# Kernel optimization log

Measured on AMD Instinct MI355X. Metric: run time of the kernel, lower is better.

## Reference

```python
import jax, jax.numpy as jnp
import numpy as np

N = 100_000      # nodes
E = 1_600_000    # edges (avg degree 16)
D_IN, D_HID, D_OUT = 64, 64, 10


def setup_inputs() -> dict:
    key = jax.random.key(0)
    ks = jax.random.split(key, 9)
    x = jax.random.normal(ks[0], (N, D_IN), jnp.float32)
    edge_index = jax.random.randint(ks[1], (2, E), 0, N, dtype=jnp.int32)

    def lin(k, i, o):
        # Glorot-ish init for a Linear(i, o) weight, stored as (in, out)
        return jax.random.normal(k, (i, o), jnp.float32) / np.sqrt(i).astype(np.float32)

    return dict(
        x=x, edge_index=edge_index,
        W_out0=lin(ks[2], D_IN, D_HID), b0=jnp.zeros((D_HID,), jnp.float32), W_root0=lin(ks[3], D_IN, D_HID),
        W_out1=lin(ks[4], D_HID, D_HID), b1=jnp.zeros((D_HID,), jnp.float32), W_root1=lin(ks[5], D_HID, D_HID),
        W_out2=lin(ks[6], D_HID, D_OUT), b2=jnp.zeros((D_OUT,), jnp.float32), W_root2=lin(ks[7], D_HID, D_OUT),
    )


def _cluster_gcn_conv(x, src, dst, deg_inv, W_out, b, W_root):
    # PyG ClusterGCNConv (add_self_loops=False, diag_lambda=0):
    #   agg[i] = (1/deg_in(i)) * sum_{(j->i) in E} x[j]
    #   out    = agg @ W_out + b + x @ W_root
    agg = jax.ops.segment_sum(x[src], dst, num_segments=N)  # [N, d]
    agg = agg * deg_inv[:, None]
    return agg @ W_out + b + x @ W_root


def reference(x, edge_index, W_out0, b0, W_root0, W_out1, b1, W_root1, W_out2, b2, W_root2):
    src, dst = edge_index[0], edge_index[1]
    deg = jax.ops.segment_sum(jnp.ones((E,), x.dtype), dst, num_segments=N)
    deg_inv = 1.0 / jnp.clip(deg, 1.0)  # degree(col).clamp_(1.)

    h = jax.nn.relu(_cluster_gcn_conv(x, src, dst, deg_inv, W_out0, b0, W_root0))
    # dropout(p=0.5) is identity in eval mode (reference uses eval semantics)
    h = jax.nn.relu(_cluster_gcn_conv(h, src, dst, deg_inv, W_out1, b1, W_root1))
    h = _cluster_gcn_conv(h, src, dst, deg_inv, W_out2, b2, W_root2)
    return jax.nn.log_softmax(h, axis=-1)
```

## Files before the change

### kernel.cpp

```cpp
#include <hip/hip_runtime.h>
#include <hip/hip_bf16.h>
#include <math.h>

#define N_NODES 100000
#define N_EDGES 1600000
#define D 64
#define DOUT 10
#define CAP 64
#define APAD 136
#define NBIN 782
#define ABLK 256
#define ACHUNK 6272
#define SCAP 32

typedef __attribute__((ext_vector_type(8))) short short8;
typedef __attribute__((ext_vector_type(4))) float f32x4;

__device__ __forceinline__ unsigned short f2bf(float f) {
    __hip_bfloat16 h = __float2bfloat16(f);
    return __builtin_bit_cast(unsigned short, h);
}
__device__ __forceinline__ float blo(unsigned v) { return __builtin_bit_cast(float, v << 16); }
__device__ __forceinline__ float bhi(unsigned v) { return __builtin_bit_cast(float, v & 0xFFFF0000u); }

#define PROCE(dv, sv) { int bin = (dv) >> 7; int r = atomicAdd(&hist[bin], 1); \
    if (r < SCAP) ebuf[((size_t)blk * NBIN + bin) * SCAP + r] = ((sv) << 7) | ((dv) & 127); }

__global__ __launch_bounds__(1024) void partA_kernel(
    const int* __restrict__ src, const int* __restrict__ dst,
    int* __restrict__ ebuf, int* __restrict__ counts,
    const float* __restrict__ x, unsigned short* __restrict__ xb,
    const float* __restrict__ W_out0, const float* __restrict__ W_root0,
    const float* __restrict__ W_out1, const float* __restrict__ W_root1,
    const float* __restrict__ W_out2, const float* __restrict__ W_root2,
    unsigned short* __restrict__ Wt0, unsigned short* __restrict__ Wt1,
    unsigned short* __restrict__ Wt2) {
    __shared__ int hist[NBIN];
    int tid = threadIdx.x;
    int blk = blockIdx.x;
    for (int i = tid; i < NBIN; i += 1024) hist[i] = 0;
    __syncthreads();
    int e0 = blk * ACHUNK;
    for (int b = tid; b < ACHUNK / 4; b += 1024) {
        int e = e0 + b * 4;
        if (e + 4 <= N_EDGES) {
            int4 d4 = *(const int4*)&dst[e];
            int4 s4 = *(const int4*)&src[e];
            PROCE(d4.x, s4.x) PROCE(d4.y, s4.y) PROCE(d4.z, s4.z) PROCE(d4.w, s4.w)
        } else {
            for (int k = 0; e + k < N_EDGES && k < 4; ++k) {
                int dv = dst[e + k], sv = src[e + k];
                PROCE(dv, sv)
            }
        }
    }
    __syncthreads();
    for (int i = tid; i < NBIN; i += 1024) {
        int h = hist[i];
        counts[blk * NBIN + i] = h < SCAP ? h : SCAP;
    }

    const int CTOT = (N_NODES + 1) * D / 4;
    for (int i = blk * 1024 + tid; i < CTOT; i += ABLK * 1024) {
        ushort4 o;
        if (i * 4 < N_NODES * D) {
            float4 v = *(const float4*)&x[i * 4];
            o.x = f2bf(v.x); o.y = f2bf(v.y); o.z = f2bf(v.z); o.w = f2bf(v.w);
        } else {
            o.x = 0; o.y = 0; o.z = 0; o.w = 0;
        }
        *(ushort4*)&xb[i * 4] = o;
    }

    for (int idx = blk * 1024 + tid; idx < 16384 + 2048; idx += ABLK * 1024) {
        if (idx < 8192) {
            int j = idx >> 7, k = idx & 127;
            Wt0[idx] = f2bf(k < 64 ? W_out0[k * D + j] : W_root0[(k - 64) * D + j]);
        } else if (idx < 16384) {
            int t = idx - 8192;
            int j = t >> 7, k = t & 127;
            Wt1[t] = f2bf(k < 64 ? W_out1[k * D + j] : W_root1[(k - 64) * D + j]);
        } else {
            int t = idx - 16384;
            int j = t >> 7, k = t & 127;
            float v = 0.f;
            if (j < DOUT) v = k < 64 ? W_out2[k * DOUT + j] : W_root2[(k - 64) * DOUT + j];
            Wt2[t] = f2bf(v);
        }
    }
}

__global__ __launch_bounds__(256) void partB_kernel(const int* __restrict__ ebuf,
                                                    const int* __restrict__ counts,
                                                    int* __restrict__ cnt,
                                                    int* __restrict__ bucket) {
    __shared__ int lb[128 * CAP];
    __shared__ int lcnt[128];
    __shared__ int sc[ABLK];
    int tid = threadIdx.x;
    int bin = blockIdx.x;
    for (int i = tid; i < 128 * CAP; i += 256) lb[i] = N_NODES;
    if (tid < 128) lcnt[tid] = 0;
    if (tid < ABLK) sc[tid] = counts[tid * NBIN + bin];
    __syncthreads();
    for (int i = tid; i < ABLK * SCAP; i += 256) {
        int seg = i >> 5;
        int slot = i & (SCAP - 1);
        if (slot < sc[seg]) {
            int v = ebuf[((size_t)seg * NBIN + bin) * SCAP + slot];
            int dloc = v & 127;
            int p = atomicAdd(&lcnt[dloc], 1);
            if (p < CAP) lb[dloc * CAP + p] = v >> 7;
        }
    }
    __syncthreads();
    size_t nodeBase = (size_t)bin << 7;
    int lastNode = N_NODES - (int)nodeBase;
    for (int i = tid; i < 128 * CAP / 4; i += 256) {
        int dloc = (i * 4) >> 6;
        if (dloc < lastNode)
            *(int4*)&bucket[nodeBase * CAP + i * 4] = *(const int4*)&lb[i * 4];
    }
    if (tid < 128 && tid < lastNode) cnt[nodeBase + tid] = lcnt[tid];
}

__global__ __launch_bounds__(256) void gather_kernel(
    const unsigned short* __restrict__ in, unsigned short* __restrict__ agg,
    const int* __restrict__ cnt, const int* __restrict__ bucket) {
    int tid = threadIdx.x;
    int lane = tid & 63;
    int g = lane >> 3, j = lane & 7;
    int wv = (blockIdx.x * blockDim.x + tid) >> 6;
    int nw = (gridDim.x * blockDim.x) >> 6;
    const int NP = (N_NODES + 8) / 8;

    for (int pr = wv; pr < NP; pr += nw) {
        int n0 = pr * 8;
        int nd = n0 + g;
        int node = nd < N_NODES ? nd : 0;
        int c = nd < N_NODES ? cnt[nd] : 0;
        int cc = c < CAP ? c : CAP;
        const int* __restrict__ brow = &bucket[(size_t)node * CAP];

        float a0 = 0.f, a1 = 0.f, a2 = 0.f, a3 = 0.f,
              a4 = 0.f, a5 = 0.f, a6 = 0.f, a7 = 0.f;
        uint4 rA = {0, 0, 0, 0}, rB = {0, 0, 0, 0}, rC = {0, 0, 0, 0};
        if (cc > 0) rA = *(const uint4*)&in[(size_t)brow[0] * D + j * 8];
        if (cc > 1) rB = *(const uint4*)&in[(size_t)brow[1] * D + j * 8];
        if (cc > 2) rC = *(const uint4*)&in[(size_t)brow[2] * D + j * 8];
        for (int it = 0; it < cc; ++it) {
            uint4 r = rA;
            rA = rB; rB = rC;
            if (it + 3 < cc) rC = *(const uint4*)&in[(size_t)brow[it + 3] * D + j * 8];
            a0 += blo(r.x); a1 += bhi(r.x);
            a2 += blo(r.y); a3 += bhi(r.y);
            a4 += blo(r.z); a5 += bhi(r.z);
            a6 += blo(r.w); a7 += bhi(r.w);
        }
        if (nd <= N_NODES) {
            float dinv = 1.0f / (float)(c > 0 ? c : 1);
            uint4 pk;
            pk.x = (unsigned)f2bf(a0 * dinv) | ((unsigned)f2bf(a1 * dinv) << 16);
            pk.y = (unsigned)f2bf(a2 * dinv) | ((unsigned)f2bf(a3 * dinv) << 16);
            pk.z = (unsigned)f2bf(a4 * dinv) | ((unsigned)f2bf(a5 * dinv) << 16);
            pk.w = (unsigned)f2bf(a6 * dinv) | ((unsigned)f2bf(a7 * dinv) << 16);
            *(uint4*)&agg[(size_t)nd * D + j * 8] = pk;
        }
    }
}

__global__ __launch_bounds__(256) void gemm_hidden_kernel(
    const unsigned short* __restrict__ agg, const unsigned short* __restrict__ xin,
    unsigned short* __restrict__ out, const unsigned short* __restrict__ Wt_g,
    const float* __restrict__ bias_v) {
    __shared__ __align__(16) unsigned short Wt[64 * APAD];
    int tid = threadIdx.x;
#pragma unroll
    for (int i = 0; i < 4; ++i) {
        int e = (tid + i * 256) * 8;
        uint4 v = *(const uint4*)&Wt_g[e];
        *(uint4*)&Wt[(e >> 7) * APAD + (e & 127)] = v;
    }
    __syncthreads();

    int lane = tid & 63, w = tid >> 6;
    int r16 = lane & 15, g4 = lane >> 4;
    int base = blockIdx.x * 64;
    int arow = base + w * 16 + r16;
    int nd = arow < N_NODES ? arow : N_NODES;

    f32x4 acc[4] = {{0.f,0.f,0.f,0.f},{0.f,0.f,0.f,0.f},{0.f,0.f,0.f,0.f},{0.f,0.f,0.f,0.f}};
#pragma unroll
    for (int ks = 0; ks < 4; ++ks) {
        int koff = ks * 32 + g4 * 8;
        short8 a;
        if (ks < 2) a = *(const short8*)&agg[(size_t)nd * D + koff];
        else        a = *(const short8*)&xin[(size_t)nd * D + (koff - 64)];
#pragma unroll
        for (int n = 0; n < 4; ++n) {
            short8 b = *(const short8*)&Wt[(n * 16 + r16) * APAD + koff];
            acc[n] = __builtin_amdgcn_mfma_f32_16x16x32_bf16(a, b, acc[n], 0, 0, 0);
        }
    }
#pragma unroll
    for (int n = 0; n < 4; ++n) {
        int col = n * 16 + r16;
        float bias = bias_v[col];
#pragma unroll
        for (int r = 0; r < 4; ++r) {
            int node = base + w * 16 + g4 * 4 + r;
            if (node <= N_NODES) {
                float v = node < N_NODES ? fmaxf(acc[n][r] + bias, 0.f) : 0.f;
                out[(size_t)node * D + col] = f2bf(v);
            }
        }
    }
}

__global__ __launch_bounds__(256) void gemm_out_kernel(
    const unsigned short* __restrict__ agg, const unsigned short* __restrict__ xin,
    float* __restrict__ out, const unsigned short* __restrict__ Wt_g,
    const float* __restrict__ bias_v) {
    __shared__ __align__(16) unsigned short Wt[16 * APAD];
    int tid = threadIdx.x;
    {
        int e = tid * 8;
        uint4 v = *(const uint4*)&Wt_g[e];
        *(uint4*)&Wt[(e >> 7) * APAD + (e & 127)] = v;
    }
    __syncthreads();

    int lane = tid & 63, w = tid >> 6;
    int r16 = lane & 15, g4 = lane >> 4;
    int base = blockIdx.x * 64;
    int arow = base + w * 16 + r16;
    int nd = arow < N_NODES ? arow : N_NODES;

    f32x4 acc = {0.f, 0.f, 0.f, 0.f};
#pragma unroll
    for (int ks = 0; ks < 4; ++ks) {
        int koff = ks * 32 + g4 * 8;
        short8 a;
        if (ks < 2) a = *(const short8*)&agg[(size_t)nd * D + koff];
        else        a = *(const short8*)&xin[(size_t)nd * D + (koff - 64)];
        short8 b = *(const short8*)&Wt[r16 * APAD + koff];
        acc = __builtin_amdgcn_mfma_f32_16x16x32_bf16(a, b, acc, 0, 0, 0);
    }
    float bias = r16 < DOUT ? bias_v[r16] : -1e30f;
#pragma unroll
    for (int r = 0; r < 4; ++r) {
        float v = acc[r] + bias;
        float m = v;
        m = fmaxf(m, __shfl_xor(m, 1, 16));
        m = fmaxf(m, __shfl_xor(m, 2, 16));
        m = fmaxf(m, __shfl_xor(m, 4, 16));
        m = fmaxf(m, __shfl_xor(m, 8, 16));
        float e = expf(v - m);
        float s = e;
        s += __shfl_xor(s, 1, 16);
        s += __shfl_xor(s, 2, 16);
        s += __shfl_xor(s, 4, 16);
        s += __shfl_xor(s, 8, 16);
        int node = base + w * 16 + g4 * 4 + r;
        if (node < N_NODES && r16 < DOUT)
            out[(size_t)node * DOUT + r16] = v - m - logf(s);
    }
}

extern "C" void kernel_launch(void* const* d_in, const int* in_sizes, int n_in,
                              void* d_out, int out_size, void* d_ws, size_t ws_size,
                              hipStream_t stream) {
    const float* x       = (const float*)d_in[0];
    const int*   ei      = (const int*)d_in[1];
    const int*   src     = ei;
    const int*   dst     = ei + N_EDGES;
    const float* W_out0  = (const float*)d_in[2];
    const float* b0      = (const float*)d_in[3];
    const float* W_root0 = (const float*)d_in[4];
    const float* W_out1  = (const float*)d_in[5];
    const float* b1      = (const float*)d_in[6];
    const float* W_root1 = (const float*)d_in[7];
    const float* W_out2  = (const float*)d_in[8];
    const float* b2      = (const float*)d_in[9];
    const float* W_root2 = (const float*)d_in[10];
    float* outp = (float*)d_out;

    const size_t ROWS = (size_t)(N_NODES + 1) * D;
    unsigned short* xb  = (unsigned short*)d_ws;
    unsigned short* h0  = xb + ROWS;
    unsigned short* h1  = h0 + ROWS;
    unsigned short* Wt0 = h1 + ROWS;
    unsigned short* Wt1 = Wt0 + 8192;
    unsigned short* Wt2 = Wt1 + 8192;
    int* cnt    = (int*)(Wt2 + 2048);
    int* bucket = cnt + N_NODES;
    int* ebuf   = bucket + (size_t)N_NODES * CAP;
    int* counts = ebuf + (size_t)ABLK * NBIN * SCAP;

    partA_kernel<<<ABLK, 1024, 0, stream>>>(src, dst, ebuf, counts, x, xb,
                                            W_out0, W_root0, W_out1, W_root1,
                                            W_out2, W_root2, Wt0, Wt1, Wt2);
    partB_kernel<<<NBIN, 256, 0, stream>>>(ebuf, counts, cnt, bucket);

    const int GB = 2048;
    const int tiles = (N_NODES + 63) / 64;
    gather_kernel<<<GB, 256, 0, stream>>>(xb, h1, cnt, bucket);
    gemm_hidden_kernel<<<tiles, 256, 0, stream>>>(h1, xb, h0, Wt0, b0);
    gather_kernel<<<GB, 256, 0, stream>>>(h0, xb, cnt, bucket);
    gemm_hidden_kernel<<<tiles, 256, 0, stream>>>(xb, h0, h1, Wt1, b1);
    gather_kernel<<<GB, 256, 0, stream>>>(h1, h0, cnt, bucket);
    gemm_out_kernel<<<tiles, 256, 0, stream>>>(h0, h1, outp, Wt2, b2);
}
```

Before: 277.3 us.

## Fuse neighbor gather into per-layer GEMM kernels via LDS staging

Merges the separate gather and GEMM kernels of each layer into one kernel per layer. Each block gathers and mean-aggregates its 64 nodes' neighbor features straight into shared memory next to the root features, then runs the MFMA GEMM from LDS. This removes the write and re-read of the intermediate aggregate buffer and three kernel launches. In exchange, the gather parallelism is tied to the GEMM tile grid (one block per 64 nodes) and each block uses more LDS, which could lower occupancy.

```diff
diff --git a/kernel.cpp b/kernel.cpp
--- a/kernel.cpp
+++ b/kernel.cpp
@@ -124,78 +124,70 @@
     if (tid < 128 && tid < lastNode) cnt[nodeBase + tid] = lcnt[tid];
 }
 
-__global__ __launch_bounds__(256) void gather_kernel(
-    const unsigned short* __restrict__ in, unsigned short* __restrict__ agg,
-    const int* __restrict__ cnt, const int* __restrict__ bucket) {
-    int tid = threadIdx.x;
-    int lane = tid & 63;
-    int g = lane >> 3, j = lane & 7;
-    int wv = (blockIdx.x * blockDim.x + tid) >> 6;
-    int nw = (gridDim.x * blockDim.x) >> 6;
-    const int NP = (N_NODES + 8) / 8;
-
-    for (int pr = wv; pr < NP; pr += nw) {
-        int n0 = pr * 8;
-        int nd = n0 + g;
-        int node = nd < N_NODES ? nd : 0;
-        int c = nd < N_NODES ? cnt[nd] : 0;
-        int cc = c < CAP ? c : CAP;
-        const int* __restrict__ brow = &bucket[(size_t)node * CAP];
-
-        float a0 = 0.f, a1 = 0.f, a2 = 0.f, a3 = 0.f,
-              a4 = 0.f, a5 = 0.f, a6 = 0.f, a7 = 0.f;
-        uint4 rA = {0, 0, 0, 0}, rB = {0, 0, 0, 0}, rC = {0, 0, 0, 0};
-        if (cc > 0) rA = *(const uint4*)&in[(size_t)brow[0] * D + j * 8];
-        if (cc > 1) rB = *(const uint4*)&in[(size_t)brow[1] * D + j * 8];
-        if (cc > 2) rC = *(const uint4*)&in[(size_t)brow[2] * D + j * 8];
-        for (int it = 0; it < cc; ++it) {
-            uint4 r = rA;
-            rA = rB; rB = rC;
-            if (it + 3 < cc) rC = *(const uint4*)&in[(size_t)brow[it + 3] * D + j * 8];
-            a0 += blo(r.x); a1 += bhi(r.x);
-            a2 += blo(r.y); a3 += bhi(r.y);
-            a4 += blo(r.z); a5 += bhi(r.z);
-            a6 += blo(r.w); a7 += bhi(r.w);
-        }
-        if (nd <= N_NODES) {
-            float dinv = 1.0f / (float)(c > 0 ? c : 1);
-            uint4 pk;
-            pk.x = (unsigned)f2bf(a0 * dinv) | ((unsigned)f2bf(a1 * dinv) << 16);
-            pk.y = (unsigned)f2bf(a2 * dinv) | ((unsigned)f2bf(a3 * dinv) << 16);
-            pk.z = (unsigned)f2bf(a4 * dinv) | ((unsigned)f2bf(a5 * dinv) << 16);
-            pk.w = (unsigned)f2bf(a6 * dinv) | ((unsigned)f2bf(a7 * dinv) << 16);
-            *(uint4*)&agg[(size_t)nd * D + j * 8] = pk;
-        }
-    }
-}
-
-__global__ __launch_bounds__(256) void gemm_hidden_kernel(
-    const unsigned short* __restrict__ agg, const unsigned short* __restrict__ xin,
-    unsigned short* __restrict__ out, const unsigned short* __restrict__ Wt_g,
-    const float* __restrict__ bias_v) {
+
+#define GATHER_TO_LDS(p)                                                              \
+    {                                                                                 \
+        int nl = w * 16 + (p) * 8 + g;                                                \
+        int nd = base + nl;                                                           \
+        int node = nd < N_NODES ? nd : 0;                                             \
+        int c = nd < N_NODES ? cnt[nd] : 0;                                           \
+        int cc = c < CAP ? c : CAP;                                                   \
+        const int* __restrict__ brow = &bucket[(size_t)node * CAP];                   \
+        float a0 = 0.f, a1 = 0.f, a2 = 0.f, a3 = 0.f,                                 \
+              a4 = 0.f, a5 = 0.f, a6 = 0.f, a7 = 0.f;                                 \
+        uint4 rA = {0,0,0,0}, rB = {0,0,0,0}, rC = {0,0,0,0};                         \
+        if (cc > 0) rA = *(const uint4*)&in[(size_t)brow[0] * D + j * 8];             \
+        if (cc > 1) rB = *(const uint4*)&in[(size_t)brow[1] * D + j * 8];             \
+        if (cc > 2) rC = *(const uint4*)&in[(size_t)brow[2] * D + j * 8];             \
+        for (int it = 0; it < cc; ++it) {                                             \
+            uint4 r = rA;                                                             \
+            rA = rB; rB = rC;                                                         \
+            if (it + 3 < cc) rC = *(const uint4*)&in[(size_t)brow[it + 3] * D + j * 8]; \
+            a0 += blo(r.x); a1 += bhi(r.x);                                           \
+            a2 += blo(r.y); a3 += bhi(r.y);                                           \
+            a4 += blo(r.z); a5 += bhi(r.z);                                           \
+            a6 += blo(r.w); a7 += bhi(r.w);                                           \
+        }                                                                             \
+        float dinv = 1.0f / (float)(c > 0 ? c : 1);                                   \
+        uint4 pk;                                                                     \
+        pk.x = (unsigned)f2bf(a0 * dinv) | ((unsigned)f2bf(a1 * dinv) << 16);         \
+        pk.y = (unsigned)f2bf(a2 * dinv) | ((unsigned)f2bf(a3 * dinv) << 16);         \
+        pk.z = (unsigned)f2bf(a4 * dinv) | ((unsigned)f2bf(a5 * dinv) << 16);         \
+        pk.w = (unsigned)f2bf(a6 * dinv) | ((unsigned)f2bf(a7 * dinv) << 16);         \
+        *(uint4*)&A[nl * APAD + j * 8] = pk;                                          \
+    }
+
+__global__ __launch_bounds__(256) void layer_fused_kernel(
+    const unsigned short* __restrict__ in, unsigned short* __restrict__ out,
+    const int* __restrict__ cnt, const int* __restrict__ bucket,
+    const unsigned short* __restrict__ Wt_g, const float* __restrict__ bias_v) {
+    __shared__ __align__(16) unsigned short A[64 * APAD];
     __shared__ __align__(16) unsigned short Wt[64 * APAD];
     int tid = threadIdx.x;
 #pragma unroll
     for (int i = 0; i < 4; ++i) {
         int e = (tid + i * 256) * 8;
-        uint4 v = *(const uint4*)&Wt_g[e];
-        *(uint4*)&Wt[(e >> 7) * APAD + (e & 127)] = v;
-    }
-    __syncthreads();
-
+        *(uint4*)&Wt[(e >> 7) * APAD + (e & 127)] = *(const uint4*)&Wt_g[e];
+    }
+    int base = blockIdx.x * 64;
+    for (int idx = tid; idx < 512; idx += 256) {
+        int r = idx >> 3, ch = idx & 7;
+        int nd = base + r; if (nd > N_NODES) nd = N_NODES;
+        *(uint4*)&A[r * APAD + D + ch * 8] = *(const uint4*)&in[(size_t)nd * D + ch * 8];
+    }
     int lane = tid & 63, w = tid >> 6;
+    int g = lane >> 3, j = lane & 7;
+    GATHER_TO_LDS(0)
+    GATHER_TO_LDS(1)
+    __syncthreads();
+
     int r16 = lane & 15, g4 = lane >> 4;
-    int base = blockIdx.x * 64;
-    int arow = base + w * 16 + r16;
-    int nd = arow < N_NODES ? arow : N_NODES;
-
+    int arow = w * 16 + r16;
     f32x4 acc[4] = {{0.f,0.f,0.f,0.f},{0.f,0.f,0.f,0.f},{0.f,0.f,0.f,0.f},{0.f,0.f,0.f,0.f}};
 #pragma unroll
     for (int ks = 0; ks < 4; ++ks) {
         int koff = ks * 32 + g4 * 8;
-        short8 a;
-        if (ks < 2) a = *(const short8*)&agg[(size_t)nd * D + koff];
-        else        a = *(const short8*)&xin[(size_t)nd * D + (koff - 64)];
+        short8 a = *(const short8*)&A[arow * APAD + koff];
 #pragma unroll
         for (int n = 0; n < 4; ++n) {
             short8 b = *(const short8*)&Wt[(n * 16 + r16) * APAD + koff];
@@ -217,32 +209,36 @@
     }
 }
 
-__global__ __launch_bounds__(256) void gemm_out_kernel(
-    const unsigned short* __restrict__ agg, const unsigned short* __restrict__ xin,
-    float* __restrict__ out, const unsigned short* __restrict__ Wt_g,
-    const float* __restrict__ bias_v) {
+__global__ __launch_bounds__(256) void layer_out_fused_kernel(
+    const unsigned short* __restrict__ in, float* __restrict__ out,
+    const int* __restrict__ cnt, const int* __restrict__ bucket,
+    const unsigned short* __restrict__ Wt_g, const float* __restrict__ bias_v) {
+    __shared__ __align__(16) unsigned short A[64 * APAD];
     __shared__ __align__(16) unsigned short Wt[16 * APAD];
     int tid = threadIdx.x;
     {
         int e = tid * 8;
-        uint4 v = *(const uint4*)&Wt_g[e];
-        *(uint4*)&Wt[(e >> 7) * APAD + (e & 127)] = v;
-    }
-    __syncthreads();
-
+        *(uint4*)&Wt[(e >> 7) * APAD + (e & 127)] = *(const uint4*)&Wt_g[e];
+    }
+    int base = blockIdx.x * 64;
+    for (int idx = tid; idx < 512; idx += 256) {
+        int r = idx >> 3, ch = idx & 7;
+        int nd = base + r; if (nd > N_NODES) nd = N_NODES;
+        *(uint4*)&A[r * APAD + D + ch * 8] = *(const uint4*)&in[(size_t)nd * D + ch * 8];
+    }
     int lane = tid & 63, w = tid >> 6;
+    int g = lane >> 3, j = lane & 7;
+    GATHER_TO_LDS(0)
+    GATHER_TO_LDS(1)
+    __syncthreads();
+
     int r16 = lane & 15, g4 = lane >> 4;
-    int base = blockIdx.x * 64;
-    int arow = base + w * 16 + r16;
-    int nd = arow < N_NODES ? arow : N_NODES;
-
+    int arow = w * 16 + r16;
     f32x4 acc = {0.f, 0.f, 0.f, 0.f};
 #pragma unroll
     for (int ks = 0; ks < 4; ++ks) {
         int koff = ks * 32 + g4 * 8;
-        short8 a;
-        if (ks < 2) a = *(const short8*)&agg[(size_t)nd * D + koff];
-        else        a = *(const short8*)&xin[(size_t)nd * D + (koff - 64)];
+        short8 a = *(const short8*)&A[arow * APAD + koff];
         short8 b = *(const short8*)&Wt[r16 * APAD + koff];
         acc = __builtin_amdgcn_mfma_f32_16x16x32_bf16(a, b, acc, 0, 0, 0);
     }
@@ -302,12 +298,8 @@
                                             W_out2, W_root2, Wt0, Wt1, Wt2);
     partB_kernel<<<NBIN, 256, 0, stream>>>(ebuf, counts, cnt, bucket);
 
-    const int GB = 2048;
     const int tiles = (N_NODES + 63) / 64;
-    gather_kernel<<<GB, 256, 0, stream>>>(xb, h1, cnt, bucket);
-    gemm_hidden_kernel<<<tiles, 256, 0, stream>>>(h1, xb, h0, Wt0, b0);
-    gather_kernel<<<GB, 256, 0, stream>>>(h0, xb, cnt, bucket);
-    gemm_hidden_kernel<<<tiles, 256, 0, stream>>>(xb, h0, h1, Wt1, b1);
-    gather_kernel<<<GB, 256, 0, stream>>>(h1, h0, cnt, bucket);
-    gemm_out_kernel<<<tiles, 256, 0, stream>>>(h0, h1, outp, Wt2, b2);
-}
+    layer_fused_kernel<<<tiles, 256, 0, stream>>>(xb, h0, cnt, bucket, Wt0, b0);
+    layer_fused_kernel<<<tiles, 256, 0, stream>>>(h0, h1, cnt, bucket, Wt1, b1);
+    layer_out_fused_kernel<<<tiles, 256, 0, stream>>>(h1, outp, cnt, bucket, Wt2, b2);
+}
```

Result: slower. 314.0 us (+13.2%).
